# Optimization experiments

Hardware: AMD Instinct MI355X
Metric: run time of the kernel (lower is better)

The kernel has to match this reference:

```python
import jax, jax.numpy as jnp
import numpy as np

NUM_GROUPS = 32
EPS = 1e-6


def setup_inputs() -> dict:
    key = jax.random.key(0)
    ks = jax.random.split(key, 6)
    b, c, H, W = 4, 512, 64, 64
    scale = 1.0 / np.sqrt(c)
    return {
        "x": jax.random.normal(ks[0], (b, c, H, W), dtype=jnp.float32),
        "gn_w": jnp.ones((c,), jnp.float32),
        "gn_b": jnp.zeros((c,), jnp.float32),
        "wq": jax.random.normal(ks[1], (c, c), jnp.float32) * scale,
        "bq": jnp.zeros((c,), jnp.float32),
        "wk": jax.random.normal(ks[2], (c, c), jnp.float32) * scale,
        "bk": jnp.zeros((c,), jnp.float32),
        "wv": jax.random.normal(ks[3], (c, c), jnp.float32) * scale,
        "bv": jnp.zeros((c,), jnp.float32),
        "wp": jax.random.normal(ks[4], (c, c), jnp.float32) * scale,
        "bp": jnp.zeros((c,), jnp.float32),
    }


def _group_norm(x, gamma, beta):
    b, c, H, W = x.shape
    xg = x.reshape(b, NUM_GROUPS, c // NUM_GROUPS, H, W)
    mean = xg.mean(axis=(2, 3, 4), keepdims=True)
    var = xg.var(axis=(2, 3, 4), keepdims=True)
    xn = (xg - mean) * jax.lax.rsqrt(var + EPS)
    xn = xn.reshape(b, c, H, W)
    return xn * gamma[None, :, None, None] + beta[None, :, None, None]


def reference(x, gn_w, gn_b, wq, bq, wk, bk, wv, bv, wp, bp):
    b, c, H, W = x.shape
    h = _group_norm(x, gn_w, gn_b)  # (b,c,H,W)
    hf = h.reshape(b, c, H * W)  # (b,c,n)
    # 1x1 convs == per-pixel linear maps; weight layout [out,in]
    q = jnp.einsum('oc,bcn->bno', wq, hf) + bq  # (b,n,c)
    k = jnp.einsum('oc,bcn->bon', wk, hf) + bk[None, :, None]  # (b,c,n)
    v = jnp.einsum('oc,bcn->bon', wv, hf) + bv[None, :, None]  # (b,c,n)
    attn = jnp.einsum('bnc,bcm->bnm', q, k) * (int(c) ** (-0.5))
    attn = jax.nn.softmax(attn, axis=2)  # softmax over keys m
    # A = v @ attn^T  -> (b,c,n) where A[:, :, n] = sum_m v[:,:,m] attn[n,m]
    A = jnp.einsum('bcm,bnm->bcn', v, attn)
    A = jnp.einsum('oc,bcn->bon', wp, A) + bp[None, :, None]
    return x + A.reshape(b, c, H, W)
```

## Files before the change

kernel.cpp:

```cpp
#include <hip/hip_runtime.h>

#define BATCH 4
#define CCH 512
#define NPIX 4096
#define NGRP 32
#define GSZ 16
#define GN_EPS 1e-6f

typedef __attribute__((ext_vector_type(8))) short short8;
typedef __attribute__((ext_vector_type(8))) unsigned short ushort8;
typedef __attribute__((ext_vector_type(4))) unsigned short ushort4v;
typedef __attribute__((ext_vector_type(4))) float f32x4;

__device__ inline unsigned short f2bf(float f) {
  unsigned u = __float_as_uint(f);
  unsigned r = u + 0x7fffu + ((u >> 16) & 1u);
  return (unsigned short)(r >> 16);
}
__device__ inline float bf2f(unsigned short us) {
  return __uint_as_float(((unsigned)us) << 16);
}

__global__ __launch_bounds__(256) void gn_stats(const float* __restrict__ x,
                                                float* __restrict__ stats) {
  int bg = blockIdx.x;
  const f32x4* base = (const f32x4*)(x + (size_t)bg * (GSZ * NPIX));
  float s = 0.f, ss = 0.f;
  const int n4 = GSZ * NPIX / 4;
  for (int i = threadIdx.x; i < n4; i += 256) {
    f32x4 v = base[i];
    s += v.x + v.y + v.z + v.w;
    ss += v.x * v.x + v.y * v.y + v.z * v.z + v.w * v.w;
  }
  for (int off = 32; off > 0; off >>= 1) {
    s += __shfl_xor(s, off, 64);
    ss += __shfl_xor(ss, off, 64);
  }
  __shared__ float rs[4], rss[4];
  int lane = threadIdx.x & 63, wid = threadIdx.x >> 6;
  if (lane == 0) { rs[wid] = s; rss[wid] = ss; }
  __syncthreads();
  if (threadIdx.x == 0) {
    float S = rs[0] + rs[1] + rs[2] + rs[3];
    float SS = rss[0] + rss[1] + rss[2] + rss[3];
    const float inv = 1.f / (float)(GSZ * NPIX);
    float mean = S * inv;
    float var = SS * inv - mean * mean;
    stats[bg * 2] = mean;
    stats[bg * 2 + 1] = rsqrtf(var + GN_EPS);
  }
}

__global__ __launch_bounds__(256) void gn_apply_t(const float* __restrict__ x,
                                                  const float* __restrict__ stats,
                                                  const float* __restrict__ gw,
                                                  const float* __restrict__ gb,
                                                  unsigned short* __restrict__ hT) {
  __shared__ float tile[64][65];
  int b = blockIdx.z, c0 = blockIdx.y * 64, n0 = blockIdx.x * 64;
  int t = threadIdx.x;
  int tc4 = t & 15, tr = t >> 4;
  const float* xb = x + ((size_t)b * CCH + c0) * NPIX + n0;
#pragma unroll
  for (int j = 0; j < 4; ++j) {
    int row = tr + j * 16;
    int c = c0 + row;
    float mean = stats[((size_t)b * NGRP + (c >> 4)) * 2];
    float rstd = stats[((size_t)b * NGRP + (c >> 4)) * 2 + 1];
    float ga = gw[c] * rstd;
    float be = gb[c] - mean * ga;
    f32x4 v = *(const f32x4*)(xb + (size_t)row * NPIX + tc4 * 4);
    tile[row][tc4 * 4 + 0] = v.x * ga + be;
    tile[row][tc4 * 4 + 1] = v.y * ga + be;
    tile[row][tc4 * 4 + 2] = v.z * ga + be;
    tile[row][tc4 * 4 + 3] = v.w * ga + be;
  }
  __syncthreads();
  int cc = t & 7, nr = t >> 3;
  unsigned short* outp = hT + ((size_t)b * NPIX + n0) * CCH + c0;
#pragma unroll
  for (int j = 0; j < 2; ++j) {
    int n = nr + j * 32;
    ushort8 pk;
#pragma unroll
    for (int i = 0; i < 8; ++i) pk[i] = f2bf(tile[cc * 8 + i][n]);
    *(ushort8*)(outp + (size_t)n * CCH + cc * 8) = pk;
  }
}

__global__ __launch_bounds__(256) void f32_to_bf16(const float* __restrict__ src,
                                                   unsigned short* __restrict__ dst,
                                                   int n4) {
  int i = blockIdx.x * 256 + threadIdx.x;
  if (i < n4) {
    f32x4 v = ((const f32x4*)src)[i];
    ushort4v o;
    o.x = f2bf(v.x); o.y = f2bf(v.y); o.z = f2bf(v.z); o.w = f2bf(v.w);
    ((ushort4v*)dst)[i] = o;
  }
}

template <int BIAS_MODE, int OUT_BF16, int RESID, int SWZ>
__global__ __launch_bounds__(256, 2) void gemm_bt(
    const unsigned short* __restrict__ A, const unsigned short* __restrict__ B,
    void* __restrict__ Cv, const float* __restrict__ bias,
    const float* __restrict__ resid, int M, int N, int K, int lda, int ldb,
    int ldc, long sA, long sB, long sC, long sR, float scale) {
  __shared__ __align__(16) unsigned short lA[128][40];
  __shared__ __align__(16) unsigned short lB[128][40];
  const int t = threadIdx.x;
  const int lane = t & 63, w = t >> 6;
  const int wr = w >> 1, wc = w & 1;
  const int fr = lane & 15, kg = lane >> 4;

  unsigned orig = blockIdx.x + gridDim.x * (blockIdx.y + gridDim.y * blockIdx.z);
  unsigned nwg = gridDim.x * gridDim.y * gridDim.z;
  unsigned tid = (orig & 7) * (nwg >> 3) + (orig >> 3);
  int mt, ntl, bz;
  if (SWZ == 2) {
    unsigned bx = tid % gridDim.x, r = tid / gridDim.x;
    ntl = (int)bx;
    mt = (int)(r % gridDim.y);
    bz = (int)(r / gridDim.y);
  } else {
    unsigned bx = tid % gridDim.x, r = tid / gridDim.x;
    mt = (int)bx;
    ntl = (int)(r % gridDim.y);
    bz = (int)(r / gridDim.y);
  }
  const int m0 = mt * 128, n0 = ntl * 128;

  const unsigned short* Abz = A + (long)bz * sA;
  const unsigned short* Bbz = B + (long)bz * sB;
  const int srow = t >> 1, skc = (t & 1) * 16;
  const unsigned short* gA = Abz + (size_t)(m0 + srow) * lda + skc;
  const unsigned short* gB = Bbz + (size_t)(n0 + srow) * ldb + skc;

  short8 a0X = *(const short8*)(gA);
  short8 a1X = *(const short8*)(gA + 8);
  short8 b0X = *(const short8*)(gB);
  short8 b1X = *(const short8*)(gB + 8);
  short8 a0Y = *(const short8*)(gA + 32);
  short8 a1Y = *(const short8*)(gA + 40);
  short8 b0Y = *(const short8*)(gB + 32);
  short8 b1Y = *(const short8*)(gB + 40);

  f32x4 acc[4][4];
  const f32x4 zero = {0.f, 0.f, 0.f, 0.f};
#pragma unroll
  for (int m = 0; m < 4; ++m)
#pragma unroll
    for (int n = 0; n < 4; ++n) acc[m][n] = zero;

  const int NT = K >> 5;
#define COMPUTE()                                                             \
  do {                                                                        \
    short8 af[4], bfr[4];                                                     \
    _Pragma("unroll") for (int m = 0; m < 4; ++m) af[m] =                     \
        *(const short8*)&lA[wr * 64 + m * 16 + fr][kg * 8];                   \
    _Pragma("unroll") for (int n = 0; n < 4; ++n) bfr[n] =                    \
        *(const short8*)&lB[wc * 64 + n * 16 + fr][kg * 8];                   \
    _Pragma("unroll") for (int m = 0; m < 4; ++m)                             \
        _Pragma("unroll") for (int n = 0; n < 4; ++n) acc[m][n] =             \
            __builtin_amdgcn_mfma_f32_16x16x32_bf16(af[m], bfr[n],            \
                                                    acc[m][n], 0, 0, 0);      \
  } while (0)

  for (int it = 0; it < NT; it += 2) {
    __syncthreads();
    *(short8*)&lA[srow][skc] = a0X;
    *(short8*)&lA[srow][skc + 8] = a1X;
    *(short8*)&lB[srow][skc] = b0X;
    *(short8*)&lB[srow][skc + 8] = b1X;
    if (it + 2 < NT) {
      a0X = *(const short8*)(gA + (it + 2) * 32);
      a1X = *(const short8*)(gA + (it + 2) * 32 + 8);
      b0X = *(const short8*)(gB + (it + 2) * 32);
      b1X = *(const short8*)(gB + (it + 2) * 32 + 8);
    }
    __syncthreads();
    COMPUTE();
    __syncthreads();
    *(short8*)&lA[srow][skc] = a0Y;
    *(short8*)&lA[srow][skc + 8] = a1Y;
    *(short8*)&lB[srow][skc] = b0Y;
    *(short8*)&lB[srow][skc + 8] = b1Y;
    if (it + 3 < NT) {
      a0Y = *(const short8*)(gA + (it + 3) * 32);
      a1Y = *(const short8*)(gA + (it + 3) * 32 + 8);
      b0Y = *(const short8*)(gB + (it + 3) * 32);
      b1Y = *(const short8*)(gB + (it + 3) * 32 + 8);
    }
    __syncthreads();
    COMPUTE();
  }
#undef COMPUTE

  const int rowbase = m0 + wr * 64 + kg * 4;
  const int colbase = n0 + wc * 64 + fr;
#pragma unroll
  for (int m = 0; m < 4; ++m) {
#pragma unroll
    for (int n = 0; n < 4; ++n) {
      int col = colbase + n * 16;
#pragma unroll
      for (int r = 0; r < 4; ++r) {
        int row = rowbase + m * 16 + r;
        float v = acc[m][n][r] * scale;
        if (BIAS_MODE == 1) v += bias[row];
        if (BIAS_MODE == 2) v += bias[col];
        if (RESID) v += resid[(size_t)bz * sR + (size_t)row * ldc + col];
        size_t idx = (size_t)bz * sC + (size_t)row * ldc + col;
        if (OUT_BF16)
          ((unsigned short*)Cv)[idx] = f2bf(v);
        else
          ((float*)Cv)[idx] = v;
      }
    }
  }
}

__global__ __launch_bounds__(512, 2) void attn_fused(
    const unsigned short* __restrict__ qg, const unsigned short* __restrict__ kgl,
    const unsigned short* __restrict__ vg, unsigned short* __restrict__ og,
    float scale) {
  __shared__ __align__(16) unsigned short Qs[64 * 512];
  __shared__ __align__(16) unsigned short Ck[2][16384];
  __shared__ __align__(16) unsigned short Ps[64 * 128];
  __shared__ float lred[2][32][4];
  __shared__ float linv[64];

  const int t = threadIdx.x;
  const int lane = t & 63;
  const int wid = t >> 6;
  const int wq = wid >> 2, wc = wid & 3;
  const int fr = lane & 15, kgp = lane >> 4;

  unsigned logical = ((unsigned)blockIdx.x & 7) * 32 + ((unsigned)blockIdx.x >> 3);
  const int bz = (int)(logical >> 6), qt = (int)(logical & 63);
  const size_t BS = (size_t)NPIX * CCH;
  const unsigned short* qb = qg + (size_t)bz * BS + (size_t)qt * 64 * CCH;
  const unsigned short* kb = kgl + (size_t)bz * BS;
  const unsigned short* vb = vg + (size_t)bz * BS;

  {
    const int row = t >> 3, c0 = (t & 7) * 64;
    const unsigned short* src = qb + (size_t)row * CCH + c0;
    const int sw = (row & 7) << 3;
#pragma unroll
    for (int i = 0; i < 8; ++i)
      *(short8*)&Qs[row * 512 + ((c0 + i * 8) ^ sw)] = *(const short8*)(src + i * 8);
  }

  const int krow = t >> 2, kseg = t & 3;
  const int kswz = (krow & 7) << 3;
  const unsigned short* gK = kb + (size_t)krow * CCH + kseg * 32;
  const unsigned short* gV = vb + (size_t)t * NPIX;

  short8 R0, R1, R2, R3;
#define LOADK(mt_, cc_)                                                       \
  do { const unsigned short* g = gK + (size_t)(mt_) * (128 * CCH) + (cc_) * 128; \
    R0 = *(const short8*)(g); R1 = *(const short8*)(g + 8);                   \
    R2 = *(const short8*)(g + 16); R3 = *(const short8*)(g + 24); } while (0)
#define LOADV(mt_, vc_)                                                       \
  do { const unsigned short* g = gV + (mt_) * 128 + (vc_) * 32;               \
    R0 = *(const short8*)(g); R1 = *(const short8*)(g + 8);                   \
    R2 = *(const short8*)(g + 16); R3 = *(const short8*)(g + 24); } while (0)
#define WRITEK(buf_)                                                          \
  do { unsigned short* d = &Ck[buf_][krow * 128];                             \
    *(short8*)(d + ((kseg * 32 + 0) ^ kswz)) = R0;                            \
    *(short8*)(d + ((kseg * 32 + 8) ^ kswz)) = R1;                            \
    *(short8*)(d + ((kseg * 32 + 16) ^ kswz)) = R2;                           \
    *(short8*)(d + ((kseg * 32 + 24) ^ kswz)) = R3; } while (0)
#define WRITEV(buf_)                                                          \
  do { unsigned short* d = &Ck[buf_][t * 8];                                  \
    *(short8*)(d + 0 * 4096) = R0; *(short8*)(d + 1 * 4096) = R1;             \
    *(short8*)(d + 2 * 4096) = R2; *(short8*)(d + 3 * 4096) = R3; } while (0)

  f32x4 oa[2][8];
  const f32x4 zero = {0.f, 0.f, 0.f, 0.f};
#pragma unroll
  for (int i = 0; i < 2; ++i)
#pragma unroll
    for (int j = 0; j < 8; ++j) oa[i][j] = zero;
  f32x4 racc0 = zero, racc1 = zero;

  LOADK(0, 0);
  for (int mt = 0; mt < 32; ++mt) {
    f32x4 s00 = zero, s01 = zero, s10 = zero, s11 = zero;
#pragma unroll
    for (int ph = 0; ph < 8; ++ph) {
      const int buf = ph & 1;
      if (ph < 4) WRITEK(buf); else WRITEV(buf);
      if (ph < 3) { LOADK(mt, ph + 1); }
      else if (ph == 3) { LOADV(mt, 0); }
      else if (ph < 7) { LOADV(mt, ph - 3); }
      else { if (mt + 1 < 32) LOADK(mt + 1, 0); }
      __syncthreads();
      if (ph < 4) {
        __builtin_amdgcn_s_setprio(1);
#pragma unroll
        for (int kk = 0; kk < 4; ++kk) {
          const int q0 = wq * 32 + fr, q1 = wq * 32 + 16 + fr;
          const int col = ph * 128 + kk * 32 + kgp * 8;
          short8 a0 = *(const short8*)&Qs[q0 * 512 + ((col) ^ ((q0 & 7) << 3))];
          short8 a1 = *(const short8*)&Qs[q1 * 512 + ((col) ^ ((q1 & 7) << 3))];
          const int m0r = wc * 32 + fr, m1r = wc * 32 + 16 + fr;
          short8 b0 = *(const short8*)&Ck[buf][m0r * 128 +
                      ((kk * 32 + kgp * 8) ^ ((m0r & 7) << 3))];
          short8 b1 = *(const short8*)&Ck[buf][m1r * 128 +
                      ((kk * 32 + kgp * 8) ^ ((m1r & 7) << 3))];
          s00 = __builtin_amdgcn_mfma_f32_16x16x32_bf16(a0, b0, s00, 0, 0, 0);
          s01 = __builtin_amdgcn_mfma_f32_16x16x32_bf16(a0, b1, s01, 0, 0, 0);
          s10 = __builtin_amdgcn_mfma_f32_16x16x32_bf16(a1, b0, s10, 0, 0, 0);
          s11 = __builtin_amdgcn_mfma_f32_16x16x32_bf16(a1, b1, s11, 0, 0, 0);
        }
        __builtin_amdgcn_s_setprio(0);
        if (ph == 3) {
          f32x4 p00, p01, p10, p11;
#pragma unroll
          for (int r = 0; r < 4; ++r) {
            p00[r] = __expf(s00[r] * scale);
            p01[r] = __expf(s01[r] * scale);
            p10[r] = __expf(s10[r] * scale);
            p11[r] = __expf(s11[r] * scale);
          }
          f32x4 rs0 = p00 + p01, rs1 = p10 + p11;
#pragma unroll
          for (int off = 1; off <= 8; off <<= 1) {
#pragma unroll
            for (int r = 0; r < 4; ++r) {
              rs0[r] += __shfl_xor(rs0[r], off, 64);
              rs1[r] += __shfl_xor(rs1[r], off, 64);
            }
          }
          racc0 += rs0;
          racc1 += rs1;
#pragma unroll
          for (int r = 0; r < 4; ++r) {
            const int qa = wq * 32 + kgp * 4 + r;
            const int qbr = wq * 32 + 16 + kgp * 4 + r;
            const int swa = (qa & 7) << 3, swb = (qbr & 7) << 3;
            Ps[qa * 128 + ((wc * 32 + fr) ^ swa)] = f2bf(p00[r]);
            Ps[qa * 128 + ((wc * 32 + 16 + fr) ^ swa)] = f2bf(p01[r]);
            Ps[qbr * 128 + ((wc * 32 + fr) ^ swb)] = f2bf(p10[r]);
            Ps[qbr * 128 + ((wc * 32 + 16 + fr) ^ swb)] = f2bf(p11[r]);
          }
        }
      } else {
        const int vc = ph - 4;
        const int q0 = wq * 32 + fr, q1 = wq * 32 + 16 + fr;
        short8 pa0 = *(const short8*)&Ps[q0 * 128 +
                     ((vc * 32 + kgp * 8) ^ ((q0 & 7) << 3))];
        short8 pa1 = *(const short8*)&Ps[q1 * 128 +
                     ((vc * 32 + kgp * 8) ^ ((q1 & 7) << 3))];
        __builtin_amdgcn_s_setprio(1);
#pragma unroll
        for (int fb = 0; fb < 8; ++fb) {
          const int c = wc * 128 + fb * 16 + fr;
          short8 bv = *(const short8*)&Ck[buf][kgp * 4096 + c * 8];
          oa[0][fb] = __builtin_amdgcn_mfma_f32_16x16x32_bf16(pa0, bv, oa[0][fb], 0, 0, 0);
          oa[1][fb] = __builtin_amdgcn_mfma_f32_16x16x32_bf16(pa1, bv, oa[1][fb], 0, 0, 0);
        }
        __builtin_amdgcn_s_setprio(0);
      }
    }
  }
#undef LOADK
#undef LOADV
#undef WRITEK
#undef WRITEV

  if (fr == 0) {
#pragma unroll
    for (int r = 0; r < 4; ++r) {
      lred[wq][kgp * 4 + r][wc] = racc0[r];
      lred[wq][16 + kgp * 4 + r][wc] = racc1[r];
    }
  }
  __syncthreads();
  if (t < 64) {
    float s = lred[t >> 5][t & 31][0] + lred[t >> 5][t & 31][1] +
              lred[t >> 5][t & 31][2] + lred[t >> 5][t & 31][3];
    linv[t] = 1.f / s;
  }
  __syncthreads();
#pragma unroll
  for (int i = 0; i < 2; ++i) {
    f32x4 li = *(const f32x4*)&linv[wq * 32 + i * 16 + kgp * 4];
#pragma unroll
    for (int fb = 0; fb < 8; ++fb) {
#pragma unroll
      for (int r = 0; r < 4; ++r) {
        const int q = wq * 32 + i * 16 + kgp * 4 + r;
        const int col = wc * 128 + fb * 16 + fr;
        Qs[q * 512 + (col ^ ((q & 7) << 3))] = f2bf(oa[i][fb][r] * li[r]);
      }
    }
  }
  __syncthreads();
  {
    const int row = t >> 3, c0 = (t & 7) * 64;
    const int sw = (row & 7) << 3;
    unsigned short* dst = og + (size_t)bz * BS + ((size_t)qt * 64 + row) * CCH + c0;
#pragma unroll
    for (int i = 0; i < 8; ++i)
      *(short8*)(dst + i * 8) = *(const short8*)&Qs[row * 512 + ((c0 + i * 8) ^ sw)];
  }
}

extern "C" void kernel_launch(void* const* d_in, const int* in_sizes, int n_in,
                              void* d_out, int out_size, void* d_ws, size_t ws_size,
                              hipStream_t stream) {
  const float* x = (const float*)d_in[0];
  const float* gnw = (const float*)d_in[1];
  const float* gnb = (const float*)d_in[2];
  const float* wq = (const float*)d_in[3];
  const float* bq = (const float*)d_in[4];
  const float* wk = (const float*)d_in[5];
  const float* bk = (const float*)d_in[6];
  const float* wv = (const float*)d_in[7];
  const float* bv = (const float*)d_in[8];
  const float* wp = (const float*)d_in[9];
  const float* bp = (const float*)d_in[10];
  float* out = (float*)d_out;

  const size_t BS = (size_t)NPIX * CCH;

  char* ws = (char*)d_ws;
  float* stats = (float*)ws;
  unsigned short* hT = (unsigned short*)(ws + 1024);
  unsigned short* Abuf = hT;
  unsigned short* qb = hT + BATCH * BS;
  unsigned short* kTb = qb + BATCH * BS;
  unsigned short* vb = kTb + BATCH * BS;
  unsigned short* wqb = vb + BATCH * BS;
  unsigned short* wkb = wqb + CCH * CCH;
  unsigned short* wvb = wkb + CCH * CCH;
  unsigned short* wpb = wvb + CCH * CCH;
  size_t need = (size_t)((char*)(wpb + CCH * CCH) - ws);
  if (ws_size < need) return;

  f32_to_bf16<<<256, 256, 0, stream>>>(wq, wqb, CCH * CCH / 4);
  f32_to_bf16<<<256, 256, 0, stream>>>(wk, wkb, CCH * CCH / 4);
  f32_to_bf16<<<256, 256, 0, stream>>>(wv, wvb, CCH * CCH / 4);
  f32_to_bf16<<<256, 256, 0, stream>>>(wp, wpb, CCH * CCH / 4);

  gn_stats<<<BATCH * NGRP, 256, 0, stream>>>(x, stats);
  gn_apply_t<<<dim3(NPIX / 64, CCH / 64, BATCH), 256, 0, stream>>>(x, stats, gnw,
                                                                   gnb, hT);

  gemm_bt<2, 1, 0, 2><<<dim3(4, 32, BATCH), 256, 0, stream>>>(
      hT, wqb, qb, bq, nullptr, NPIX, CCH, CCH, CCH, CCH, CCH, (long)BS, 0,
      (long)BS, 0, 1.f);
  gemm_bt<2, 1, 0, 2><<<dim3(4, 32, BATCH), 256, 0, stream>>>(
      hT, wkb, kTb, bk, nullptr, NPIX, CCH, CCH, CCH, CCH, CCH, (long)BS, 0,
      (long)BS, 0, 1.f);
  gemm_bt<1, 1, 0, 0><<<dim3(4, 32, BATCH), 256, 0, stream>>>(
      wvb, hT, vb, bv, nullptr, CCH, NPIX, CCH, CCH, CCH, NPIX, 0, (long)BS,
      (long)BS, 0, 1.f);

  const float sscale = 0.044194173824159216f;
  attn_fused<<<BATCH * 64, 512, 0, stream>>>(qb, kTb, vb, Abuf, sscale);

  gemm_bt<1, 0, 1, 0><<<dim3(4, 32, BATCH), 256, 0, stream>>>(
      wpb, Abuf, out, bp, x, CCH, NPIX, CCH, CCH, CCH, NPIX, 0, (long)BS,
      (long)BS, (long)BS, 1.f);
}
```

Baseline: 338.2 us.

## Stream K and V tiles directly into LDS with global_load_lds

Replaces the register-staged K/V copy (global load into VGPRs, then a swizzled LDS write) with async `global_load_lds` 16-byte transfers. These are issued right after each barrier into the other LDS buffer. Per-lane source addresses are remapped so the existing XOR swizzle and V layout in LDS stay the same. This removes the LDS write instructions and the staging registers, and lets loads overlap the MFMA work on the current buffer. In exchange, prefetch depth is now one phase issued after the barrier, and correctness depends on the barrier waiting for the outstanding vector-memory loads.

New measurement: 422.0 us. 1.25x slower.

```diff
diff --git a/kernel.cpp b/kernel.cpp
--- a/kernel.cpp
+++ b/kernel.cpp
@@ -20,6 +20,11 @@
 __device__ inline float bf2f(unsigned short us) {
   return __uint_as_float(((unsigned)us) << 16);
 }
+
+#define GLOAD16(g, l)                                                         \
+  __builtin_amdgcn_global_load_lds(                                           \
+      (__attribute__((address_space(1))) void*)(g),                           \
+      (__attribute__((address_space(3))) void*)(l), 16, 0, 0)
 
 __global__ __launch_bounds__(256) void gn_stats(const float* __restrict__ x,
                                                 float* __restrict__ stats) {
@@ -243,6 +248,44 @@
   const unsigned short* kb = kgl + (size_t)bz * BS;
   const unsigned short* vb = vg + (size_t)bz * BS;
 
+  const int ldsE = wid * 2048 + lane * 8;
+  const int rlo = lane >> 4, g15 = lane & 15;
+  const unsigned short* kS0 =
+      kb + (size_t)((wid * 4 + 0) * 4 + rlo) * CCH + ((g15 ^ rlo) << 3);
+  const unsigned short* kS1 =
+      kb + (size_t)((wid * 4 + 1) * 4 + rlo) * CCH + ((g15 ^ (4 + rlo)) << 3);
+  const unsigned short* kS2 =
+      kb + (size_t)((wid * 4 + 2) * 4 + rlo) * CCH + ((g15 ^ rlo) << 3);
+  const unsigned short* kS3 =
+      kb + (size_t)((wid * 4 + 3) * 4 + rlo) * CCH + ((g15 ^ (4 + rlo)) << 3);
+#define VSRCP(i)                                                              \
+  (vb + (size_t)((((wid * 4 + (i)) & 7) * 64) + lane) * NPIX +                \
+   (((wid * 4 + (i)) >> 3) << 3))
+  const unsigned short* vS0 = VSRCP(0);
+  const unsigned short* vS1 = VSRCP(1);
+  const unsigned short* vS2 = VSRCP(2);
+  const unsigned short* vS3 = VSRCP(3);
+#undef VSRCP
+
+#define ISSUE_K(BUF, mt_, sub_)                                               \
+  do {                                                                        \
+    const long o = (long)(mt_) * (128 * CCH) + (long)(sub_)*128;              \
+    GLOAD16(kS0 + o, &Ck[BUF][ldsE]);                                         \
+    GLOAD16(kS1 + o, &Ck[BUF][ldsE + 512]);                                   \
+    GLOAD16(kS2 + o, &Ck[BUF][ldsE + 1024]);                                  \
+    GLOAD16(kS3 + o, &Ck[BUF][ldsE + 1536]);                                  \
+  } while (0)
+
+#define ISSUE_V(BUF, mt_, vc_)                                                \
+  do {                                                                        \
+    const long o = (long)(mt_)*128 + (long)(vc_)*32;                          \
+    GLOAD16(vS0 + o, &Ck[BUF][ldsE]);                                         \
+    GLOAD16(vS1 + o, &Ck[BUF][ldsE + 512]);                                   \
+    GLOAD16(vS2 + o, &Ck[BUF][ldsE + 1024]);                                  \
+    GLOAD16(vS3 + o, &Ck[BUF][ldsE + 1536]);                                  \
+  } while (0)
+
+  ISSUE_K(0, 0, 0);
   {
     const int row = t >> 3, c0 = (t & 7) * 64;
     const unsigned short* src = qb + (size_t)row * CCH + c0;
@@ -252,31 +295,6 @@
       *(short8*)&Qs[row * 512 + ((c0 + i * 8) ^ sw)] = *(const short8*)(src + i * 8);
   }
 
-  const int krow = t >> 2, kseg = t & 3;
-  const int kswz = (krow & 7) << 3;
-  const unsigned short* gK = kb + (size_t)krow * CCH + kseg * 32;
-  const unsigned short* gV = vb + (size_t)t * NPIX;
-
-  short8 R0, R1, R2, R3;
-#define LOADK(mt_, cc_)                                                       \
-  do { const unsigned short* g = gK + (size_t)(mt_) * (128 * CCH) + (cc_) * 128; \
-    R0 = *(const short8*)(g); R1 = *(const short8*)(g + 8);                   \
-    R2 = *(const short8*)(g + 16); R3 = *(const short8*)(g + 24); } while (0)
-#define LOADV(mt_, vc_)                                                       \
-  do { const unsigned short* g = gV + (mt_) * 128 + (vc_) * 32;               \
-    R0 = *(const short8*)(g); R1 = *(const short8*)(g + 8);                   \
-    R2 = *(const short8*)(g + 16); R3 = *(const short8*)(g + 24); } while (0)
-#define WRITEK(buf_)                                                          \
-  do { unsigned short* d = &Ck[buf_][krow * 128];                             \
-    *(short8*)(d + ((kseg * 32 + 0) ^ kswz)) = R0;                            \
-    *(short8*)(d + ((kseg * 32 + 8) ^ kswz)) = R1;                            \
-    *(short8*)(d + ((kseg * 32 + 16) ^ kswz)) = R2;                           \
-    *(short8*)(d + ((kseg * 32 + 24) ^ kswz)) = R3; } while (0)
-#define WRITEV(buf_)                                                          \
-  do { unsigned short* d = &Ck[buf_][t * 8];                                  \
-    *(short8*)(d + 0 * 4096) = R0; *(short8*)(d + 1 * 4096) = R1;             \
-    *(short8*)(d + 2 * 4096) = R2; *(short8*)(d + 3 * 4096) = R3; } while (0)
-
   f32x4 oa[2][8];
   const f32x4 zero = {0.f, 0.f, 0.f, 0.f};
 #pragma unroll
@@ -285,18 +303,17 @@
     for (int j = 0; j < 8; ++j) oa[i][j] = zero;
   f32x4 racc0 = zero, racc1 = zero;
 
-  LOADK(0, 0);
   for (int mt = 0; mt < 32; ++mt) {
     f32x4 s00 = zero, s01 = zero, s10 = zero, s11 = zero;
 #pragma unroll
     for (int ph = 0; ph < 8; ++ph) {
       const int buf = ph & 1;
-      if (ph < 4) WRITEK(buf); else WRITEV(buf);
-      if (ph < 3) { LOADK(mt, ph + 1); }
-      else if (ph == 3) { LOADV(mt, 0); }
-      else if (ph < 7) { LOADV(mt, ph - 3); }
-      else { if (mt + 1 < 32) LOADK(mt + 1, 0); }
       __syncthreads();
+      if (ph < 3)       ISSUE_K(buf ^ 1, mt, ph + 1);
+      else if (ph == 3) ISSUE_V(buf ^ 1, mt, 0);
+      else if (ph < 7)  ISSUE_V(buf ^ 1, mt, ph - 3);
+      else if (mt + 1 < 32) ISSUE_K(buf ^ 1, mt + 1, 0);
+      __builtin_amdgcn_sched_barrier(0);
       if (ph < 4) {
         __builtin_amdgcn_s_setprio(1);
 #pragma unroll
@@ -346,6 +363,7 @@
             Ps[qbr * 128 + ((wc * 32 + fr) ^ swb)] = f2bf(p10[r]);
             Ps[qbr * 128 + ((wc * 32 + 16 + fr) ^ swb)] = f2bf(p11[r]);
           }
+          s00 = zero; s01 = zero; s10 = zero; s11 = zero;
         }
       } else {
         const int vc = ph - 4;
@@ -366,11 +384,10 @@
       }
     }
   }
-#undef LOADK
-#undef LOADV
-#undef WRITEK
-#undef WRITEV
-
+#undef ISSUE_K
+#undef ISSUE_V
+
+  __syncthreads();
   if (fr == 0) {
 #pragma unroll
     for (int r = 0; r < 4; ++r) {
```
